# Kernel optimization log

Measured on AMD Instinct MI355X. Metric: run time of the kernel, lower is better.

## Reference

```python
import jax, jax.numpy as jnp
import numpy as np

N_U = 50000; N_I = 50000; F = 128; H = 128; E = 800000; G = 512; C = 16; L = 3
EPS = 1e-5


def setup_inputs() -> dict:
    key = jax.random.key(0)
    ks = jax.random.split(key, 22)
    s = 1.0 / np.sqrt(H)
    inp = {}
    inp["x_user"] = jax.random.normal(ks[0], (N_U, F), jnp.float32)
    inp["x_item"] = jax.random.normal(ks[1], (N_I, F), jnp.float32)
    inp["edge_u2i"] = jnp.stack([jax.random.randint(ks[2], (E,), 0, N_U),
                                 jax.random.randint(ks[3], (E,), 0, N_I)])
    inp["edge_i2u"] = jnp.stack([jax.random.randint(ks[4], (E,), 0, N_I),
                                 jax.random.randint(ks[5], (E,), 0, N_U)])
    inp["batch_user"] = jnp.sort(jax.random.randint(ks[6], (N_U,), 0, G))
    inp["batch_item"] = jnp.sort(jax.random.randint(ks[7], (N_I,), 0, G))
    # GraphConv params per layer per relation (in-dim == hidden == 128, so stackable)
    inp["Wrel_u2i"] = jax.random.uniform(ks[8], (L, H, F), jnp.float32, -s, s)
    inp["Wroot_u2i"] = jax.random.uniform(ks[9], (L, H, F), jnp.float32, -s, s)
    inp["b_u2i"] = jax.random.uniform(ks[10], (L, H), jnp.float32, -s, s)
    inp["Wrel_i2u"] = jax.random.uniform(ks[11], (L, H, F), jnp.float32, -s, s)
    inp["Wroot_i2u"] = jax.random.uniform(ks[12], (L, H, F), jnp.float32, -s, s)
    inp["b_i2u"] = jax.random.uniform(ks[13], (L, H), jnp.float32, -s, s)
    # BatchNorm (one module per node type, reused across layers)
    inp["bn_g_user"] = jnp.ones((H,), jnp.float32)
    inp["bn_b_user"] = jnp.zeros((H,), jnp.float32)
    inp["bn_g_item"] = jnp.ones((H,), jnp.float32)
    inp["bn_b_item"] = jnp.zeros((H,), jnp.float32)
    # per-layer classifier heads
    inp["fc_W"] = jax.random.uniform(ks[14], (L, C, H), jnp.float32, -s, s)
    inp["fc_b"] = jax.random.uniform(ks[15], (L, C), jnp.float32, -s, s)
    return inp


def _graph_conv(x_src, x_dst, edge, Wrel, Wroot, b, n_dst):
    # GraphConv, aggr='add': W_rel @ sum_{j in N(i)} x_j + W_root @ x_i + b
    agg = jax.ops.segment_sum(x_src[edge[0]], edge[1], num_segments=n_dst)  # [n_dst, F]
    return agg @ Wrel.T + x_dst @ Wroot.T + b


def _bn(x, g, b):
    # BatchNorm1d over nodes, training-mode batch statistics (biased var)
    m = x.mean(0)
    v = jnp.mean((x - m) ** 2, axis=0)
    return (x - m) * jax.lax.rsqrt(v + EPS) * g + b


def reference(x_user, x_item, edge_u2i, edge_i2u, batch_user, batch_item,
              Wrel_u2i, Wroot_u2i, b_u2i, Wrel_i2u, Wroot_i2u, b_i2u,
              bn_g_user, bn_b_user, bn_g_item, bn_b_item, fc_W, fc_b):
    batch_all = jnp.concatenate([batch_user, batch_item])
    cnt = jax.ops.segment_sum(jnp.ones((N_U + N_I,), jnp.float32), batch_all,
                              num_segments=G)
    cnt = jnp.maximum(cnt, 1.0)[:, None]
    feats = []
    xu, xi = x_user, x_item
    for l in range(L):
        new_i = _graph_conv(xu, xi, edge_u2i, Wrel_u2i[l], Wroot_u2i[l], b_u2i[l], N_I)
        new_u = _graph_conv(xi, xu, edge_i2u, Wrel_i2u[l], Wroot_i2u[l], b_i2u[l], N_U)
        xu = _bn(jax.nn.relu(new_u), bn_g_user, bn_b_user)
        xi = _bn(jax.nn.relu(new_i), bn_g_item, bn_b_item)
        pooled = jax.ops.segment_sum(jnp.concatenate([xu, xi], 0), batch_all,
                                     num_segments=G) / cnt  # global mean pool [G, H]
        feats.append(pooled)
    feats = jnp.stack(feats)  # [L, G, H]
    # eval mode: F.dropout is identity; per-layer linear heads
    logits = jnp.einsum('lgh,lch->lgc', feats, fc_W) + fc_b[:, None, :]  # [L, G, C]
    return (logits, feats)
```

## Files before the change

### kernel.cpp

```cpp
#include <hip/hip_runtime.h>

#define NN 50000
#define FD 128
#define NE 800000
#define NG 512
#define NC 16
#define NL 3
#define NTOT 100000
#define NBLK 391
#define NBUCK 196
#define CAP 10240
#define BINTILE 2048
#define NBINBLK 782
#define BNEPS 1e-5f
#define LOGITS_N (NL*NG*NC)
#define Q4 800000

typedef unsigned short u16;
typedef unsigned char u8;
typedef __attribute__((ext_vector_type(8))) short short8;
typedef __attribute__((ext_vector_type(4))) float f32x4;

#define OFF_GCNT     0ul
#define OFF_BCUR     4096ul
#define OFF_ACC      5120ul
#define MEMSET_BYTES 9216ul
#define OFF_USTART   9728ul
#define OFF_ISTART   12288ul
#define OFF_INVCNT   14848ul
#define OFF_ROWRANGE 16896ul
#define OFF_WB       817152ul
#define OFF_CSR      1210368ul
#define OFF_N0I      9238528ul
#define OFF_N0U      22038528ul
#define OFF_P        34838528ul
#define OFF_WBS      35362816ul
#define OFF_BVEC     35493888ul
#define OFF_XU0      60438528ul
#define OFF_XI0      73238528ul

static __device__ __forceinline__ float bf2f(u16 v) {
  return __uint_as_float(((unsigned)v) << 16);
}
static __device__ __forceinline__ u16 f2bf(float f) {
  unsigned u = __float_as_uint(f);
  return (u16)((u + 0x7FFFu + ((u >> 16) & 1u)) >> 16);
}
template<int RELU>
static __device__ __forceinline__ void accT8(float* a, int4 v) {
  unsigned w[4] = {(unsigned)v.x, (unsigned)v.y, (unsigned)v.z, (unsigned)v.w};
  #pragma unroll
  for (int i = 0; i < 4; i++) {
    float lo = __uint_as_float(w[i] << 16);
    float hi = __uint_as_float(w[i] & 0xffff0000u);
    if (RELU) { lo = lo > 0.f ? lo : 0.f; hi = hi > 0.f ? hi : 0.f; }
    a[2*i]   += lo;
    a[2*i+1] += hi;
  }
}
static __device__ __forceinline__ int relu2(int w) {
  int lo = (w & 0x00008000) ? 0 : (w & 0x0000FFFF);
  int hi = (w < 0)          ? 0 : (int)(w & 0xFFFF0000u);
  return lo | hi;
}
static __device__ __forceinline__ ushort4 cvt4(float4 v) {
  ushort4 o = { f2bf(v.x), f2bf(v.y), f2bf(v.z), f2bf(v.w) };
  return o;
}

__global__ __launch_bounds__(256) void k_bin(const int* __restrict__ eu2i,
                                             const int* __restrict__ ei2u,
                                             int* __restrict__ bcursor,
                                             int* __restrict__ binned,
                                             const int* __restrict__ bu,
                                             const int* __restrict__ bi,
                                             int* __restrict__ gcnt) {
  if (blockIdx.x >= NBINBLK) {
    int i = (blockIdx.x - NBINBLK)*256 + threadIdx.x;
    int lane = threadIdx.x & 63;
    bool valid = i < NTOT;
    int slot = -1;
    if (valid) {
      int type = i >= NN;
      int g = type ? bi[i-NN] : bu[i];
      slot = type*NG + g;
    }
    int prevslot = __shfl_up(slot, 1);
    bool head = valid && (lane == 0 || prevslot != slot);
    unsigned long long hb = __ballot(head);
    int nvalid = __popcll(__ballot(valid));
    if (head) {
      unsigned long long higher = (lane < 63) ? (hb >> (lane+1)) : 0ull;
      int next = higher ? (lane + __ffsll(higher)) : 64;
      int end = next < nvalid ? next : nvalid;
      atomicAdd(&gcnt[slot], end - lane);
    }
    return;
  }
  __shared__ int hist[256];
  __shared__ int scan[256];
  __shared__ int gbase[256];
  __shared__ int rbuf[BINTILE];
  __shared__ u8 rbk[BINTILE];
  int tid = threadIdx.x;
  int base = blockIdx.x * BINTILE;
  hist[tid] = 0;
  __syncthreads();
  int packr[8], bkr[8], rankr[8];
  #pragma unroll
  for (int c = 0; c < 8; c++) {
    int idx = base + c*256 + tid;
    if (idx < 2*NE) {
      int rel = idx >= NE;
      int e = rel ? idx - NE : idx;
      const int* edge = rel ? ei2u : eu2i;
      int s = edge[e];
      int d = edge[NE + e];
      int slot = d + (rel ? NN : 0);
      int bk = slot >> 9;
      bkr[c] = bk;
      packr[c] = ((slot & 511) << 17) | s;
      rankr[c] = atomicAdd(&hist[bk], 1);
    } else bkr[c] = -1;
  }
  __syncthreads();
  scan[tid] = hist[tid];
  __syncthreads();
  for (int o = 1; o < 256; o <<= 1) {
    int v = (tid >= o) ? scan[tid - o] : 0;
    __syncthreads();
    scan[tid] += v;
    __syncthreads();
  }
  if (tid < NBUCK && hist[tid] > 0)
    gbase[tid] = atomicAdd(&bcursor[tid], hist[tid]);
  __syncthreads();
  #pragma unroll
  for (int c = 0; c < 8; c++) {
    if (bkr[c] >= 0) {
      int bk = bkr[c];
      int lpos = scan[bk] - hist[bk] + rankr[c];
      rbuf[lpos] = packr[c];
      rbk[lpos] = (u8)bk;
    }
  }
  __syncthreads();
  int nv = min(BINTILE, 2*NE - base);
  for (int j = tid; j < nv; j += 256) {
    int bk = rbk[j];
    int outpos = bk*CAP + gbase[bk] + (j - (scan[bk] - hist[bk]));
    binned[outpos] = rbuf[j];
  }
}

__global__ __launch_bounds__(256) void k_csrbuild(const int* __restrict__ bcursor,
                                                  int* __restrict__ csrbin,
                                                  int2* __restrict__ rowrange,
                                                  const int* __restrict__ gcnt,
                                                  int* __restrict__ ustart,
                                                  int* __restrict__ istart,
                                                  float* __restrict__ invcnt) {
  __shared__ int lcnt[512];
  __shared__ int scan2[256];
  __shared__ int lcsr[CAP];
  int b = blockIdx.x;
  int tid = threadIdx.x;
  if (b == NBUCK) {
    int cu0 = gcnt[2*tid],     cu1 = gcnt[2*tid + 1];
    int ci0 = gcnt[NG + 2*tid], ci1 = gcnt[NG + 2*tid + 1];
    int su = cu0 + cu1, si = ci0 + ci1;
    lcnt[tid] = su; lcsr[tid] = si;
    __syncthreads();
    for (int o = 1; o < 256; o <<= 1) {
      int vu = (tid >= o) ? lcnt[tid - o] : 0;
      int vi = (tid >= o) ? lcsr[tid - o] : 0;
      __syncthreads();
      lcnt[tid] += vu; lcsr[tid] += vi;
      __syncthreads();
    }
    int eu = lcnt[tid] - su;
    int ei = lcsr[tid] - si;
    ustart[2*tid]     = eu;        ustart[2*tid + 1] = eu + cu0;
    istart[2*tid]     = ei;        istart[2*tid + 1] = ei + ci0;
    if (tid == 255) { ustart[NG] = lcnt[255]; istart[NG] = lcsr[255]; }
    int c0 = cu0 + ci0, c1 = cu1 + ci1;
    invcnt[2*tid]     = 1.0f / (float)(c0 > 0 ? c0 : 1);
    invcnt[2*tid + 1] = 1.0f / (float)(c1 > 0 ? c1 : 1);
    return;
  }
  int slot0 = b << 9;
  int nslots = min(512, NTOT - slot0);
  int n = bcursor[b];
  int gb = b * CAP;
  lcnt[tid] = 0; lcnt[tid + 256] = 0;
  __syncthreads();
  for (int i = tid; i < n; i += 256) {
    int e = csrbin[gb + i];
    atomicAdd(&lcnt[e >> 17], 1);
  }
  __syncthreads();
  int v0 = lcnt[2*tid], v1 = lcnt[2*tid + 1];
  int ps = v0 + v1;
  scan2[tid] = ps;
  __syncthreads();
  for (int o = 1; o < 256; o <<= 1) {
    int v = (tid >= o) ? scan2[tid - o] : 0;
    __syncthreads();
    scan2[tid] += v;
    __syncthreads();
  }
  int e0 = scan2[tid] - ps;
  int e1 = e0 + v0;
  if (2*tid < nslots)     rowrange[slot0 + 2*tid]     = make_int2(gb + e0, gb + e0 + v0);
  if (2*tid + 1 < nslots) rowrange[slot0 + 2*tid + 1] = make_int2(gb + e1, gb + e1 + v1);
  __syncthreads();
  lcnt[2*tid] = e0; lcnt[2*tid + 1] = e1;
  __syncthreads();
  for (int i = tid; i < n; i += 256) {
    int e = csrbin[gb + i];
    int pos = atomicAdd(&lcnt[e >> 17], 1);
    lcsr[pos] = e & 0x1FFFF;
  }
  __syncthreads();
  for (int i = tid; i < n; i += 256) csrbin[gb + i] = lcsr[i];
}

__global__ __launch_bounds__(256) void k_cast(const float* __restrict__ xu,
                                              const float* __restrict__ xi,
                                              u16* __restrict__ xbu,
                                              u16* __restrict__ xbi,
                                              const float* __restrict__ WrelA,
                                              const float* __restrict__ WrootA,
                                              const float* __restrict__ WrelB,
                                              const float* __restrict__ WrootB,
                                              u16* __restrict__ WB,
                                              float* __restrict__ P) {
  int b = blockIdx.x;
  if (b < 3125) {
    int t = b*256 + threadIdx.x;
    const float4* su = (const float4*)xu;
    const float4* si = (const float4*)xi;
    float4 v0 = su[t];
    float4 v1 = su[t + Q4];
    float4 v2 = si[t];
    float4 v3 = si[t + Q4];
    ushort4* du = (ushort4*)xbu;
    ushort4* di = (ushort4*)xbi;
    du[t]      = cvt4(v0);
    du[t + Q4] = cvt4(v1);
    di[t]      = cvt4(v2);
    di[t + Q4] = cvt4(v3);
  } else if (b < 3381) {
    int idx = (b - 3125)*256 + threadIdx.x;
    int lr = idx >> 15;
    int rem = idx & 32767;
    int h = rem >> 8;
    int k = rem & 255;
    int rel = lr & 1;
    const float* Wr = rel ? WrelB : WrelA;
    const float* Wo = rel ? WrootB : WrootA;
    float v = (k < FD) ? Wr[h*FD + k] : Wo[h*FD + (k-FD)];
    WB[idx] = f2bf(v);
  } else {
    int idx = (b - 3381)*256 + threadIdx.x;
    P[idx] = 0.f;
  }
}

__global__ __launch_bounds__(256) void k_bnfold2(const float* __restrict__ WrelA,
                                                 const float* __restrict__ WrootA,
                                                 const float* __restrict__ WrelB,
                                                 const float* __restrict__ WrootB,
                                                 int l,
                                                 const float* __restrict__ accSQ,
                                                 float* __restrict__ accSQz,
                                                 const float* __restrict__ gu,
                                                 const float* __restrict__ bu_,
                                                 const float* __restrict__ gi_,
                                                 const float* __restrict__ bi_,
                                                 u16* __restrict__ WBs,
                                                 float* __restrict__ bvec,
                                                 float* __restrict__ P,
                                                 const int* __restrict__ ustart,
                                                 const int* __restrict__ istart,
                                                 const float* __restrict__ invcnt,
                                                 float* __restrict__ feats,
                                                 int mode) {
  __shared__ float sc_l[256], sh_l[256];
  int tid = threadIdx.x;
  {
    int type = tid >> 7;
    int c = tid & 127;
    float s = accSQ[tid];
    float q = accSQ[256 + tid];
    float inv = 1.0f / (float)NN;
    float mean = s * inv;
    float var = q * inv - mean*mean;
    float rstd = rsqrtf(var + BNEPS);
    float g = type ? gi_[c] : gu[c];
    float bb = type ? bi_[c] : bu_[c];
    float sc = rstd * g;
    sc_l[tid] = sc;
    sh_l[tid] = bb - mean * sc;
  }
  __syncthreads();
  int b = blockIdx.x;
  int nfold = mode ? 0 : 66;
  if (b < nfold) {
    if (b < 64) {
      int e = b*256 + tid;
      int rel = e >> 13;
      int rem = e & 8191;
      int h = rem >> 6;
      int k0 = (rem & 63) * 4;
      const float* Wr = rel ? WrelB : WrelA;
      const float* Wo = rel ? WrootB : WrootA;
      const float* scs = sc_l + (rel ? 128 : 0);
      const float* scd = sc_l + (rel ? 0 : 128);
      u16 t[4];
      #pragma unroll
      for (int j = 0; j < 4; j++) {
        int k = k0 + j;
        float v = (k < FD) ? Wr[((size_t)l*FD + h)*FD + k] * scs[k]
                           : Wo[((size_t)l*FD + h)*FD + (k - FD)] * scd[k - FD];
        t[j] = f2bf(v);
      }
      ushort4 o = { t[0], t[1], t[2], t[3] };
      *(ushort4*)(WBs + rel*32768 + h*256 + k0) = o;
    } else {
      int vid = (b - 64)*256 + tid;
      int kind = vid >> 8;
      int rel = (vid >> 7) & 1;
      int h = vid & 127;
      const float* W = kind ? (rel ? WrootB : WrootA) : (rel ? WrelB : WrelA);
      const float* sh = sh_l + ((kind ^ rel) ? 128 : 0);
      const float* wrow = W + ((size_t)l*FD + h)*FD;
      float s = 0.f;
      #pragma unroll
      for (int k = 0; k < FD; k += 4) {
        float4 wv = *(const float4*)(wrow + k);
        float4 sv = { sh[k], sh[k+1], sh[k+2], sh[k+3] };
        s += wv.x*sv.x + wv.y*sv.y + wv.z*sv.z + wv.w*sv.w;
      }
      bvec[kind*256 + rel*128 + h] = s;
    }
  } else {
    int fb = b - nfold;
    if (fb == 0) { accSQz[tid] = 0.f; accSQz[256 + tid] = 0.f; }
    int g = fb*2 + (tid >> 7);
    int ch = tid & 127;
    size_t iu = (size_t)g*FD + ch;
    size_t ii = (size_t)NG*FD + iu;
    float pu = P[iu];
    float pi = P[ii];
    float cu = (float)(ustart[g+1] - ustart[g]);
    float ci = (float)(istart[g+1] - istart[g]);
    feats[iu] = invcnt[g] * (sc_l[ch]*pu + cu*sh_l[ch]
                           + sc_l[128+ch]*pi + ci*sh_l[128+ch]);
    P[iu] = 0.f; P[ii] = 0.f;
  }
}

template<int RELU>
__global__ __launch_bounds__(256) void k_gather(const u16* __restrict__ curU,
                                                const u16* __restrict__ curI,
                                                const int2* __restrict__ rowrange,
                                                const int* __restrict__ csr,
                                                u16* __restrict__ aggI,
                                                u16* __restrict__ aggU) {
  int b = blockIdx.x;
  int half = b >= 12500;
  int blk = half ? b - 12500 : b;
  const u16* src = half ? curI : curU;
  u16* out = half ? aggU : aggI;
  int slotbase = half ? NN : 0;
  int wid = __builtin_amdgcn_readfirstlane(threadIdx.x >> 6);
  int row = blk*4 + wid;
  int lane = threadIdx.x & 63;
  int q = lane >> 4;
  int c16 = (lane & 15) * 8;
  const u16* sp = src + c16;
  int2 pr = rowrange[slotbase + row];
  int p = pr.x, pe = pr.y;
  float a0[8], a1[8];
  #pragma unroll
  for (int j = 0; j < 8; j++) { a0[j] = 0.f; a1[j] = 0.f; }
  if (p + 8 <= pe) {
    int i0 = csr[p + q], i1 = csr[p + 4 + q];
    while (p + 16 <= pe) {
      int n0 = csr[p + 8 + q], n1 = csr[p + 12 + q];
      int4 v0 = *(const int4*)(sp + (size_t)i0*FD);
      int4 v1 = *(const int4*)(sp + (size_t)i1*FD);
      accT8<RELU>(a0, v0); accT8<RELU>(a1, v1);
      i0 = n0; i1 = n1; p += 8;
    }
    int4 v0 = *(const int4*)(sp + (size_t)i0*FD);
    int4 v1 = *(const int4*)(sp + (size_t)i1*FD);
    accT8<RELU>(a0, v0); accT8<RELU>(a1, v1);
    p += 8;
  }
  int rem = pe - p;
  if (q < rem) {
    int s = csr[p + q];
    accT8<RELU>(a0, *(const int4*)(sp + (size_t)s*FD));
  }
  if (q + 4 < rem) {
    int s = csr[p + 4 + q];
    accT8<RELU>(a1, *(const int4*)(sp + (size_t)s*FD));
  }
  #pragma unroll
  for (int j = 0; j < 8; j++) a0[j] += a1[j];
  #pragma unroll
  for (int j = 0; j < 8; j++) {
    a0[j] += __shfl_xor(a0[j], 16);
    a0[j] += __shfl_xor(a0[j], 32);
  }
  if (q == 0) {
    int4 o;
    o.x = (unsigned)f2bf(a0[0]) | ((unsigned)f2bf(a0[1]) << 16);
    o.y = (unsigned)f2bf(a0[2]) | ((unsigned)f2bf(a0[3]) << 16);
    o.z = (unsigned)f2bf(a0[4]) | ((unsigned)f2bf(a0[5]) << 16);
    o.w = (unsigned)f2bf(a0[6]) | ((unsigned)f2bf(a0[7]) << 16);
    *(int4*)(out + (size_t)row*FD + c16) = o;
  }
}

__global__ __launch_bounds__(256) void k_gemm(u16* __restrict__ newU,
                                              u16* __restrict__ newI,
                                              const u16* __restrict__ curU,
                                              const u16* __restrict__ curI,
                                              const u16* __restrict__ WBl,
                                              const float* __restrict__ bI2U,
                                              const float* __restrict__ bU2I,
                                              float* __restrict__ accSQ,
                                              const float* __restrict__ bvec,
                                              const int2* __restrict__ rowrange,
                                              const int* __restrict__ bu,
                                              const int* __restrict__ bi,
                                              const int* __restrict__ ustart,
                                              const int* __restrict__ istart,
                                              float* __restrict__ P,
                                              int fold) {
  __shared__ u16 smem[128*72*2];
  __shared__ float Sred[2][4][128];
  u16* As = smem;
  u16* Bs = smem + 128*72;
  u16* Cs = smem;
  int ty = blockIdx.y;
  u16* A1 = ty ? newI : newU;
  const u16* A2 = ty ? curI : curU;
  const u16* WBp = ty ? WBl : (WBl + 32768);
  const float* bias = ty ? bU2I : bI2U;
  const float* b1p = bvec + (ty ? 0 : 128);
  const float* b2p = bvec + 256 + (ty ? 0 : 128);
  const int* batch = ty ? bi : bu;
  const int* st = ty ? istart : ustart;
  float* Pg = P + (size_t)ty*NG*FD;
  int slot0 = ty ? 0 : NN;
  int tid = threadIdx.x;
  int n0 = blockIdx.x * 128;
  int w = __builtin_amdgcn_readfirstlane(tid >> 6);
  int lane = tid & 63;
  int l15 = lane & 15;
  int quad = lane >> 4;
  f32x4 acc[2][8];
  #pragma unroll
  for (int tr = 0; tr < 2; tr++)
    #pragma unroll
    for (int tc = 0; tc < 8; tc++)
      acc[tr][tc] = (f32x4){0.f,0.f,0.f,0.f};

  for (int ch = 0; ch < 4; ch++) {
    const u16* Ap = (ch < 2) ? ((const u16*)A1 + ch*64) : (A2 + (ch-2)*64);
    int dorelu = fold && (ch >= 2);
    #pragma unroll
    for (int i = 0; i < 4; i++) {
      int e = i*256 + tid;
      int r = e >> 3, seg = e & 7;
      int4 v = {0,0,0,0};
      int gr = n0 + r;
      if (gr < NN) v = *(const int4*)(Ap + (size_t)gr*FD + seg*8);
      if (dorelu) { v.x = relu2(v.x); v.y = relu2(v.y); v.z = relu2(v.z); v.w = relu2(v.w); }
      *(int4*)&As[r*72 + seg*8] = v;
    }
    #pragma unroll
    for (int i = 0; i < 4; i++) {
      int e = i*256 + tid;
      int r = e >> 3, seg = e & 7;
      int4 v = *(const int4*)(WBp + r*256 + ch*64 + seg*8);
      *(int4*)&Bs[r*72 + seg*8] = v;
    }
    __syncthreads();
    #pragma unroll
    for (int ks = 0; ks < 2; ks++) {
      int kb = ks*32 + quad*8;
      short8 af0 = *(const short8*)&As[(w*32 + l15)*72 + kb];
      short8 af1 = *(const short8*)&As[(w*32 + 16 + l15)*72 + kb];
      short8 bf[8];
      #pragma unroll
      for (int tc = 0; tc < 8; tc++)
        bf[tc] = *(const short8*)&Bs[(tc*16 + l15)*72 + kb];
      #pragma unroll
      for (int tc = 0; tc < 8; tc++) {
        acc[0][tc] = __builtin_amdgcn_mfma_f32_16x16x32_bf16(af0, bf[tc], acc[0][tc], 0, 0, 0);
        acc[1][tc] = __builtin_amdgcn_mfma_f32_16x16x32_bf16(af1, bf[tc], acc[1][tc], 0, 0, 0);
      }
    }
    __syncthreads();
  }
  float sv[8], qv[8], bj[8], b1j[8];
  #pragma unroll
  for (int tc = 0; tc < 8; tc++) {
    int col = tc*16 + l15;
    float base = bias[col];
    if (fold) { base += b2p[col]; b1j[tc] = b1p[col]; } else b1j[tc] = 0.f;
    bj[tc] = base;
    sv[tc] = 0.f; qv[tc] = 0.f;
  }
  float dg[2][4] = {{0.f,0.f,0.f,0.f},{0.f,0.f,0.f,0.f}};
  if (fold) {
    #pragma unroll
    for (int tr = 0; tr < 2; tr++)
      #pragma unroll
      for (int gq = 0; gq < 4; gq++) {
        int r = n0 + w*32 + tr*16 + quad*4 + gq;
        if (r < NN) {
          int2 rr = rowrange[slot0 + r];
          dg[tr][gq] = (float)(rr.y - rr.x);
        }
      }
  }
  #pragma unroll
  for (int tr = 0; tr < 2; tr++) {
    int rl0 = w*32 + tr*16 + quad*4;
    int rbase = n0 + rl0;
    #pragma unroll
    for (int tc = 0; tc < 8; tc++) {
      int col = tc*16 + l15;
      #pragma unroll
      for (int g = 0; g < 4; g++) {
        int r = rbase + g;
        float v = acc[tr][tc][g] + bj[tc] + dg[tr][g]*b1j[tc];
        Cs[(rl0 + g)*132 + col] = f2bf(v);
        if (r < NN) {
          float y = v > 0.f ? v : 0.f;
          sv[tc] += y; qv[tc] += y*y;
        }
      }
    }
  }
  #pragma unroll
  for (int tc = 0; tc < 8; tc++) {
    sv[tc] += __shfl_xor(sv[tc], 16); qv[tc] += __shfl_xor(qv[tc], 16);
    sv[tc] += __shfl_xor(sv[tc], 32); qv[tc] += __shfl_xor(qv[tc], 32);
  }
  if (quad == 0) {
    #pragma unroll
    for (int tc = 0; tc < 8; tc++) {
      Sred[0][w][tc*16 + l15] = sv[tc];
      Sred[1][w][tc*16 + l15] = qv[tc];
    }
  }
  __syncthreads();
  if (tid < 128) {
    float s = Sred[0][0][tid] + Sred[0][1][tid] + Sred[0][2][tid] + Sred[0][3][tid];
    float q = Sred[1][0][tid] + Sred[1][1][tid] + Sred[1][2][tid] + Sred[1][3][tid];
    atomicAdd(&accSQ[ty*128 + tid], s);
    atomicAdd(&accSQ[256 + ty*128 + tid], q);
  }
  {
    int col = tid & 127;
    int half = tid >> 7;
    int rlo = half * 64, rhi = rlo + 64;
    int gg0 = batch[n0];
    int lastr = n0 + 127; if (lastr > NN - 1) lastr = NN - 1;
    int gg1 = batch[lastr];
    for (int g = gg0; g <= gg1; ++g) {
      int lo = st[g]   - n0; lo = lo < rlo ? rlo : lo;
      int hi = st[g+1] - n0; hi = hi > rhi ? rhi : hi;
      float s = 0.f;
      for (int r = lo; r < hi; ++r) {
        float v = bf2f(Cs[r*132 + col]);
        s += v > 0.f ? v : 0.f;
      }
      if (hi > lo) atomicAdd(&Pg[(size_t)g*FD + col], s);
    }
  }
  int prow = tid >> 4;
  int pc = (tid & 15) * 8;
  #pragma unroll
  for (int j = 0; j < 8; j++) {
    int row = j*16 + prow;
    int gr = n0 + row;
    int4 vv = *(const int4*)&Cs[row*132 + pc];
    if (gr < NN) *(int4*)(A1 + (size_t)gr*FD + pc) = vv;
  }
}

__global__ __launch_bounds__(256) void k_heads(const float* __restrict__ feats,
                                               const float* __restrict__ fcW,
                                               const float* __restrict__ fcb,
                                               float* __restrict__ logits) {
  int idx = blockIdx.x*256 + threadIdx.x;
  if (idx >= LOGITS_N) return;
  int l = idx >> 13;
  int rem = idx & 8191;
  int g = rem >> 4;
  int c = rem & 15;
  const float* f = feats + ((size_t)l*NG + g)*FD;
  const float* w = fcW + ((size_t)l*NC + c)*FD;
  float s = 0.f;
  #pragma unroll
  for (int k = 0; k < FD; k += 4) {
    float4 fv = *(const float4*)(f + k);
    float4 wv = *(const float4*)(w + k);
    s += fv.x*wv.x + fv.y*wv.y + fv.z*wv.z + fv.w*wv.w;
  }
  logits[idx] = s + fcb[l*NC + c];
}

extern "C" void kernel_launch(void* const* d_in, const int* in_sizes, int n_in,
                              void* d_out, int out_size, void* d_ws, size_t ws_size,
                              hipStream_t stream) {
  const float* x_user   = (const float*)d_in[0];
  const float* x_item   = (const float*)d_in[1];
  const int*   eu2i     = (const int*)d_in[2];
  const int*   ei2u     = (const int*)d_in[3];
  const int*   bu       = (const int*)d_in[4];
  const int*   bi       = (const int*)d_in[5];
  const float* Wrel_u2i = (const float*)d_in[6];
  const float* Wroot_u2i= (const float*)d_in[7];
  const float* b_u2i    = (const float*)d_in[8];
  const float* Wrel_i2u = (const float*)d_in[9];
  const float* Wroot_i2u= (const float*)d_in[10];
  const float* b_i2u    = (const float*)d_in[11];
  const float* bn_g_user= (const float*)d_in[12];
  const float* bn_b_user= (const float*)d_in[13];
  const float* bn_g_item= (const float*)d_in[14];
  const float* bn_b_item= (const float*)d_in[15];
  const float* fcW      = (const float*)d_in[16];
  const float* fcb      = (const float*)d_in[17];

  char* ws = (char*)d_ws;
  int*   gcnt   = (int*)(ws + OFF_GCNT);
  int*   bcursor= (int*)(ws + OFF_BCUR);
  float* accSQ  = (float*)(ws + OFF_ACC);
  int*   ustart = (int*)(ws + OFF_USTART);
  int*   istart = (int*)(ws + OFF_ISTART);
  float* invcnt = (float*)(ws + OFF_INVCNT);
  int2*  rowrange = (int2*)(ws + OFF_ROWRANGE);
  u16*   WB     = (u16*)(ws + OFF_WB);
  int*   csrbin = (int*)(ws + OFF_CSR);
  u16*   p0I    = (u16*)(ws + OFF_N0I);
  u16*   p0U    = (u16*)(ws + OFF_N0U);
  float* P      = (float*)(ws + OFF_P);
  u16*   WBs    = (u16*)(ws + OFF_WBS);
  float* bvec   = (float*)(ws + OFF_BVEC);
  u16*   p1U    = (u16*)(ws + OFF_XU0);
  u16*   p1I    = (u16*)(ws + OFF_XI0);
  float* fout   = (float*)d_out;
  float* featsAll = fout + LOGITS_N;

  float* bank0 = accSQ;
  float* bank1 = accSQ + 512;

  hipMemsetAsync(ws, 0, MEMSET_BYTES, stream);
  k_bin<<<NBINBLK + 391, 256, 0, stream>>>(eu2i, ei2u, bcursor, csrbin,
                                           bu, bi, gcnt);
  k_csrbuild<<<NBUCK + 1, 256, 0, stream>>>(bcursor, csrbin, rowrange,
                                            gcnt, ustart, istart, invcnt);
  k_cast<<<3893, 256, 0, stream>>>(x_user, x_item, p1U, p1I,
                                   Wrel_u2i, Wroot_u2i, Wrel_i2u, Wroot_i2u,
                                   WB, P);

  k_gather<0><<<25000, 256, 0, stream>>>(p1U, p1I, rowrange, csrbin, p0I, p0U);
  k_gemm<<<dim3(NBLK,2), 256, 0, stream>>>(p0U, p0I, p1U, p1I, WB,
                                           b_i2u, b_u2i, bank0,
                                           bvec, rowrange, bu, bi,
                                           ustart, istart, P, 0);
  k_bnfold2<<<322, 256, 0, stream>>>(Wrel_u2i, Wroot_u2i, Wrel_i2u, Wroot_i2u,
                                     1, bank0, bank1,
                                     bn_g_user, bn_b_user, bn_g_item, bn_b_item,
                                     WBs, bvec, P, ustart, istart, invcnt,
                                     featsAll, 0);

  k_gather<1><<<25000, 256, 0, stream>>>(p0U, p0I, rowrange, csrbin, p1I, p1U);
  k_gemm<<<dim3(NBLK,2), 256, 0, stream>>>(p1U, p1I, p0U, p0I, WBs,
                                           b_i2u + FD, b_u2i + FD, bank1,
                                           bvec, rowrange, bu, bi,
                                           ustart, istart, P, 1);
  k_bnfold2<<<322, 256, 0, stream>>>(Wrel_u2i, Wroot_u2i, Wrel_i2u, Wroot_i2u,
                                     2, bank1, bank0,
                                     bn_g_user, bn_b_user, bn_g_item, bn_b_item,
                                     WBs, bvec, P, ustart, istart, invcnt,
                                     featsAll + NG*FD, 0);

  k_gather<1><<<25000, 256, 0, stream>>>(p1U, p1I, rowrange, csrbin, p0I, p0U);
  k_gemm<<<dim3(NBLK,2), 256, 0, stream>>>(p0U, p0I, p1U, p1I, WBs,
                                           b_i2u + 2*FD, b_u2i + 2*FD, bank0,
                                           bvec, rowrange, bu, bi,
                                           ustart, istart, P, 1);
  k_bnfold2<<<256, 256, 0, stream>>>(Wrel_u2i, Wroot_u2i, Wrel_i2u, Wroot_i2u,
                                     2, bank0, bank1,
                                     bn_g_user, bn_b_user, bn_g_item, bn_b_item,
                                     WBs, bvec, P, ustart, istart, invcnt,
                                     featsAll + 2*NG*FD, 1);

  k_heads<<<96, 256, 0, stream>>>(featsAll, fcW, fcb, fout);
}
```

Baseline: 468.2 us.

## Fuse classifier heads into BN fold kernel and prefetch GEMM A tiles into registers

Removes the separate k_heads launch by computing each layer's logits inside the pooled-feature branch of k_bnfold2, using a shared-memory copy of the two graphs' features. Also software-pipelines the A-operand loads in k_gemm: the next chunk is loaded into registers after the barrier, overlapping with the MFMA loop. Adds a min-blocks launch bound of 4 on k_gemm, which caps registers per thread. The register prefetch and the occupancy hint may cause spills, and the in-kernel head computation runs on only 32 threads per block.

```diff
diff --git a/kernel.cpp b/kernel.cpp
--- a/kernel.cpp
+++ b/kernel.cpp
@@ -285,8 +285,12 @@
                                                  const int* __restrict__ istart,
                                                  const float* __restrict__ invcnt,
                                                  float* __restrict__ feats,
+                                                 const float* __restrict__ fcWl,
+                                                 const float* __restrict__ fcbl,
+                                                 float* __restrict__ logitsl,
                                                  int mode) {
   __shared__ float sc_l[256], sh_l[256];
+  __shared__ float ft[2][128];
   int tid = threadIdx.x;
   {
     int type = tid >> 7;
@@ -347,7 +351,8 @@
   } else {
     int fb = b - nfold;
     if (fb == 0) { accSQz[tid] = 0.f; accSQz[256 + tid] = 0.f; }
-    int g = fb*2 + (tid >> 7);
+    int g2 = tid >> 7;
+    int g = fb*2 + g2;
     int ch = tid & 127;
     size_t iu = (size_t)g*FD + ch;
     size_t ii = (size_t)NG*FD + iu;
@@ -355,9 +360,25 @@
     float pi = P[ii];
     float cu = (float)(ustart[g+1] - ustart[g]);
     float ci = (float)(istart[g+1] - istart[g]);
-    feats[iu] = invcnt[g] * (sc_l[ch]*pu + cu*sh_l[ch]
-                           + sc_l[128+ch]*pi + ci*sh_l[128+ch]);
+    float fv = invcnt[g] * (sc_l[ch]*pu + cu*sh_l[ch]
+                          + sc_l[128+ch]*pi + ci*sh_l[128+ch]);
+    feats[iu] = fv;
+    ft[g2][ch] = fv;
     P[iu] = 0.f; P[ii] = 0.f;
+    __syncthreads();
+    if (tid < 32) {
+      int gg = tid >> 4;
+      int c = tid & 15;
+      const float* wrow = fcWl + (size_t)c*FD;
+      float s = 0.f;
+      #pragma unroll
+      for (int k = 0; k < FD; k += 4) {
+        float4 wv = *(const float4*)(wrow + k);
+        s += ft[gg][k]*wv.x + ft[gg][k+1]*wv.y
+           + ft[gg][k+2]*wv.z + ft[gg][k+3]*wv.w;
+      }
+      logitsl[(size_t)(fb*2 + gg)*NC + c] = s + fcbl[c];
+    }
   }
 }
 
@@ -425,7 +446,7 @@
   }
 }
 
-__global__ __launch_bounds__(256) void k_gemm(u16* __restrict__ newU,
+__global__ __launch_bounds__(256, 4) void k_gemm(u16* __restrict__ newU,
                                               u16* __restrict__ newI,
                                               const u16* __restrict__ curU,
                                               const u16* __restrict__ curI,
@@ -470,16 +491,26 @@
     for (int tc = 0; tc < 8; tc++)
       acc[tr][tc] = (f32x4){0.f,0.f,0.f,0.f};
 
+  int4 aR[4];
+  {
+    const u16* Ap = (const u16*)A1;
+    #pragma unroll
+    for (int i = 0; i < 4; i++) {
+      int e = i*256 + tid;
+      int r = e >> 3, seg = e & 7;
+      int gr = n0 + r;
+      int4 v = {0,0,0,0};
+      if (gr < NN) v = *(const int4*)(Ap + (size_t)gr*FD + seg*8);
+      aR[i] = v;
+    }
+  }
   for (int ch = 0; ch < 4; ch++) {
-    const u16* Ap = (ch < 2) ? ((const u16*)A1 + ch*64) : (A2 + (ch-2)*64);
     int dorelu = fold && (ch >= 2);
     #pragma unroll
     for (int i = 0; i < 4; i++) {
       int e = i*256 + tid;
       int r = e >> 3, seg = e & 7;
-      int4 v = {0,0,0,0};
-      int gr = n0 + r;
-      if (gr < NN) v = *(const int4*)(Ap + (size_t)gr*FD + seg*8);
+      int4 v = aR[i];
       if (dorelu) { v.x = relu2(v.x); v.y = relu2(v.y); v.z = relu2(v.z); v.w = relu2(v.w); }
       *(int4*)&As[r*72 + seg*8] = v;
     }
@@ -491,6 +522,19 @@
       *(int4*)&Bs[r*72 + seg*8] = v;
     }
     __syncthreads();
+    if (ch < 3) {
+      const u16* Apn = (ch + 1 < 2) ? ((const u16*)A1 + (ch+1)*64)
+                                    : (A2 + (ch-1)*64);
+      #pragma unroll
+      for (int i = 0; i < 4; i++) {
+        int e = i*256 + tid;
+        int r = e >> 3, seg = e & 7;
+        int gr = n0 + r;
+        int4 v = {0,0,0,0};
+        if (gr < NN) v = *(const int4*)(Apn + (size_t)gr*FD + seg*8);
+        aR[i] = v;
+      }
+    }
     #pragma unroll
     for (int ks = 0; ks < 2; ks++) {
       int kb = ks*32 + quad*8;
@@ -595,28 +639,6 @@
     int4 vv = *(const int4*)&Cs[row*132 + pc];
     if (gr < NN) *(int4*)(A1 + (size_t)gr*FD + pc) = vv;
   }
-}
-
-__global__ __launch_bounds__(256) void k_heads(const float* __restrict__ feats,
-                                               const float* __restrict__ fcW,
-                                               const float* __restrict__ fcb,
-                                               float* __restrict__ logits) {
-  int idx = blockIdx.x*256 + threadIdx.x;
-  if (idx >= LOGITS_N) return;
-  int l = idx >> 13;
-  int rem = idx & 8191;
-  int g = rem >> 4;
-  int c = rem & 15;
-  const float* f = feats + ((size_t)l*NG + g)*FD;
-  const float* w = fcW + ((size_t)l*NC + c)*FD;
-  float s = 0.f;
-  #pragma unroll
-  for (int k = 0; k < FD; k += 4) {
-    float4 fv = *(const float4*)(f + k);
-    float4 wv = *(const float4*)(w + k);
-    s += fv.x*wv.x + fv.y*wv.y + fv.z*wv.z + fv.w*wv.w;
-  }
-  logits[idx] = s + fcb[l*NC + c];
 }
 
 extern "C" void kernel_launch(void* const* d_in, const int* in_sizes, int n_in,
@@ -682,7 +704,7 @@
                                      1, bank0, bank1,
                                      bn_g_user, bn_b_user, bn_g_item, bn_b_item,
                                      WBs, bvec, P, ustart, istart, invcnt,
-                                     featsAll, 0);
+                                     featsAll, fcW, fcb, fout, 0);
 
   k_gather<1><<<25000, 256, 0, stream>>>(p0U, p0I, rowrange, csrbin, p1I, p1U);
   k_gemm<<<dim3(NBLK,2), 256, 0, stream>>>(p1U, p1I, p0U, p0I, WBs,
@@ -693,7 +715,8 @@
                                      2, bank1, bank0,
                                      bn_g_user, bn_b_user, bn_g_item, bn_b_item,
                                      WBs, bvec, P, ustart, istart, invcnt,
-                                     featsAll + NG*FD, 0);
+                                     featsAll + NG*FD,
+                                     fcW + NC*FD, fcb + NC, fout + NG*NC, 0);
 
   k_gather<1><<<25000, 256, 0, stream>>>(p1U, p1I, rowrange, csrbin, p0I, p0U);
   k_gemm<<<dim3(NBLK,2), 256, 0, stream>>>(p0U, p0I, p1U, p1I, WBs,
@@ -704,7 +727,6 @@
                                      2, bank0, bank1,
                                      bn_g_user, bn_b_user, bn_g_item, bn_b_item,
                                      WBs, bvec, P, ustart, istart, invcnt,
-                                     featsAll + 2*NG*FD, 1);
-
-  k_heads<<<96, 256, 0, stream>>>(featsAll, fcW, fcb, fout);
-}
+                                     featsAll + 2*NG*FD,
+                                     fcW + 2*NC*FD, fcb + 2*NC, fout + 2*NG*NC, 1);
+}
```

Measured after the change: 446.4 us. -4.6%, faster.
